# Performance work log

Hardware: AMD Instinct MI355X
Metric: run time of the kernel (lower is better)

## Reference

```python
import jax, jax.numpy as jnp
import numpy as np

B, L, H, T = 32, 512, 768, 8  # batch, tokens, dim_hidden, num_trees
DK = H // T


def setup_inputs() -> dict:
    key = jax.random.key(0)
    ks = jax.random.split(key, 8)
    s = 1.0 / np.sqrt(H)
    return {
        "input": jax.random.normal(ks[0], (B, L, H), dtype=jnp.float32),
        "src_mask": jax.random.randint(ks[1], (B, L), 0, 2, dtype=jnp.int32),
        "Wq": jax.random.uniform(ks[2], (H, H), minval=-s, maxval=s, dtype=jnp.float32),
        "bq": jax.random.uniform(ks[3], (H,), minval=-s, maxval=s, dtype=jnp.float32),
        "Wk": jax.random.uniform(ks[4], (H, H), minval=-s, maxval=s, dtype=jnp.float32),
        "bk": jax.random.uniform(ks[5], (H,), minval=-s, maxval=s, dtype=jnp.float32),
        "Wroot": jax.random.uniform(ks[6], (T, H), minval=-s, maxval=s, dtype=jnp.float32),
        "broot": jax.random.uniform(ks[7], (T,), minval=-s, maxval=s, dtype=jnp.float32),
    }


def reference(input, src_mask, Wq, bq, Wk, bk, Wroot, broot):
    x = input
    # multi-head attention probabilities (eval mode, no dropout)
    q = (x @ Wq.T + bq).reshape(B, L, T, DK).transpose(0, 2, 1, 3)  # (B,T,L,DK)
    k = (x @ Wk.T + bk).reshape(B, L, T, DK).transpose(0, 2, 1, 3)
    scores = jnp.einsum("btqd,btkd->btqk", q, k) / jnp.sqrt(jnp.float32(DK))
    scores = jnp.where(src_mask[:, None, None, :] == 0, -1e9, scores)
    p_attn = jax.nn.softmax(scores, axis=-1)  # (B,T,L,L) == f_ij per tree

    # root scores f_i per tree: (B,T,L)
    f = jnp.einsum("blh,th->btl", x, Wroot) + broot[None, :, None]

    eye = jnp.eye(L, dtype=x.dtype)
    A = jnp.exp(p_attn) * (1.0 - eye)           # zero diagonal
    deg = A.sum(axis=2)                          # column sums (dim=1 per tree)
    Lap = -A + deg[..., None, :] * eye           # Laplacian, deg on diagonal
    Lbar = Lap.at[:, :, 0, :].set(f)             # replace first row with root scores

    LLinv = jnp.linalg.inv(Lbar)                 # (B,T,L,L)
    d0 = f * LLinv[..., 0]                       # f_i * LLinv[:, :, 0]  -> (B,T,L)
    diag = jnp.diagonal(LLinv, axis1=-2, axis2=-1)  # (B,T,L)
    tmp1 = A * diag[..., None, :]                # A[i,j] * LLinv[j,j]
    tmp2 = A * jnp.swapaxes(LLinv, -1, -2)       # A[i,j] * LLinv[j,i]
    col_mask = (jnp.arange(L) != 0).astype(x.dtype)[None, None, None, :]  # zero first col
    row_mask = (jnp.arange(L) != 0).astype(x.dtype)[None, None, :, None]  # zero first row
    dx = col_mask * tmp1 - row_mask * tmp2       # (B,T,L,L)

    d = jnp.concatenate([d0[..., None, :], dx], axis=-2)  # (B,T,L+1,L)
    df = jnp.swapaxes(d, -1, -2)                 # (B,T,L,L+1)
    att = df[..., 1:]                            # (B,T,L,L); stacked adj_list
    return att
```

## Files before the change

### kernel.cpp

```cpp
#include <hip/hip_runtime.h>
#include <math.h>

#define NB_ 64
#define NPH 8

__global__ __launch_bounds__(256) void proj_gemm(const float* __restrict__ x,
    const float* __restrict__ Wq, const float* __restrict__ bq,
    const float* __restrict__ Wk, const float* __restrict__ bk,
    float* __restrict__ Qb, float* __restrict__ Kb) {
  const float* W    = blockIdx.z ? Wk : Wq;
  const float* bias = blockIdx.z ? bk : bq;
  float* out        = blockIdx.z ? Kb : Qb;
  const int m0 = blockIdx.x * 128;
  const int n0 = blockIdx.y * 64;
  __shared__ float Xs[16][132];
  __shared__ float Ws[16][68];
  const int tid = threadIdx.x;
  const int tm = tid & 15, tn = tid >> 4;
  float acc[8][4];
#pragma unroll
  for (int i = 0; i < 8; i++)
#pragma unroll
    for (int j = 0; j < 4; j++) acc[i][j] = 0.f;

  for (int kk = 0; kk < 768; kk += 16) {
#pragma unroll
    for (int rep = 0; rep < 2; rep++) {
      int fidx = tid + rep * 256;
      int row = fidx >> 2, f4i = fidx & 3;
      float4 v = ((const float4*)(x + (size_t)(m0 + row) * 768 + kk))[f4i];
      Xs[f4i * 4 + 0][row] = v.x; Xs[f4i * 4 + 1][row] = v.y;
      Xs[f4i * 4 + 2][row] = v.z; Xs[f4i * 4 + 3][row] = v.w;
    }
    { int row = tid >> 2, f4i = tid & 3;
      float4 v = ((const float4*)(W + (size_t)(n0 + row) * 768 + kk))[f4i];
      Ws[f4i * 4 + 0][row] = v.x; Ws[f4i * 4 + 1][row] = v.y;
      Ws[f4i * 4 + 2][row] = v.z; Ws[f4i * 4 + 3][row] = v.w;
    }
    __syncthreads();
#pragma unroll
    for (int k = 0; k < 16; k++) {
      float4 a0 = *(const float4*)&Xs[k][tm * 4];
      float4 a1 = *(const float4*)&Xs[k][tm * 4 + 64];
      float4 bv = *(const float4*)&Ws[k][tn * 4];
      float am[8] = {a0.x,a0.y,a0.z,a0.w,a1.x,a1.y,a1.z,a1.w};
      float bn[4] = {bv.x,bv.y,bv.z,bv.w};
#pragma unroll
      for (int i = 0; i < 8; i++)
#pragma unroll
        for (int j = 0; j < 4; j++) acc[i][j] += am[i] * bn[j];
    }
    __syncthreads();
  }
  float b0 = bias[n0 + tn * 4 + 0], b1 = bias[n0 + tn * 4 + 1];
  float b2 = bias[n0 + tn * 4 + 2], b3 = bias[n0 + tn * 4 + 3];
#pragma unroll
  for (int i = 0; i < 4; i++) {
    float4 o = {acc[i][0] + b0, acc[i][1] + b1, acc[i][2] + b2, acc[i][3] + b3};
    *(float4*)(out + (size_t)(m0 + tm * 4 + i) * 768 + n0 + tn * 4) = o;
    float4 o2 = {acc[i+4][0] + b0, acc[i+4][1] + b1, acc[i+4][2] + b2, acc[i+4][3] + b3};
    *(float4*)(out + (size_t)(m0 + 64 + tm * 4 + i) * 768 + n0 + tn * 4) = o2;
  }
}

__global__ __launch_bounds__(256) void f_kernel(const float* __restrict__ x,
    const float* __restrict__ Wroot, const float* __restrict__ broot,
    float* __restrict__ fout) {
  int row = blockIdx.x * 256 + threadIdx.x;
  int b = row >> 9, l = row & 511;
  float acc[8] = {0,0,0,0,0,0,0,0};
  const float4* xr = (const float4*)(x + (size_t)row * 768);
  for (int h4 = 0; h4 < 192; h4++) {
    float4 xv = xr[h4];
#pragma unroll
    for (int t = 0; t < 8; t++) {
      float4 wv = ((const float4*)(Wroot + (size_t)t * 768))[h4];
      acc[t] += xv.x * wv.x + xv.y * wv.y + xv.z * wv.z + xv.w * wv.w;
    }
  }
#pragma unroll
  for (int t = 0; t < 8; t++)
    fout[(size_t)((b * 8 + t) << 9) + l] = acc[t] + broot[t];
}

__global__ __launch_bounds__(256) void scores_kernel(const float* __restrict__ Qb,
    const float* __restrict__ Kb, const int* __restrict__ mask,
    float* __restrict__ A) {
  const int lin = blockIdx.x;
  const int xcd = lin & 7;
  const int idx = lin >> 3;
  const int bt  = xcd * 32 + (idx >> 5);
  const int q0  = (idx & 31) * 16;
  const int b = bt >> 3, t = bt & 7;
  __shared__ float  S[16][512];
  __shared__ float4 Qs4[16][24];
  __shared__ float  part[16][16];
  __shared__ float  invsum[16];
  const int tid = threadIdx.x;
  for (int i = tid; i < 384; i += 256) {
    int q = i / 24, f4 = i % 24;
    Qs4[q][f4] =
        ((const float4*)(Qb + (size_t)(b * 512 + q0 + q) * 768 + t * 96))[f4];
  }
  __syncthreads();
  const float scl = 0.10206207261596575f;
#pragma unroll 1
  for (int rep = 0; rep < 2; rep++) {
    const int k = rep * 256 + tid;
    const float4* kr = (const float4*)(Kb + (size_t)(b * 512 + k) * 768 + t * 96);
    float acc[16];
#pragma unroll
    for (int q = 0; q < 16; q++) acc[q] = 0.f;
#pragma unroll 4
    for (int f4 = 0; f4 < 24; f4++) {
      float4 kv = kr[f4];
#pragma unroll
      for (int q = 0; q < 16; q++) {
        float4 qv = Qs4[q][f4];
        acc[q] += qv.x * kv.x + qv.y * kv.y + qv.z * kv.z + qv.w * kv.w;
      }
    }
    int mk = mask[b * 512 + k];
#pragma unroll
    for (int q = 0; q < 16; q++)
      S[q][k] = mk ? expf(acc[q] * scl) : 0.f;
  }
  __syncthreads();
  { int q = tid >> 4, j = tid & 15;
    float s = 0.f;
#pragma unroll
    for (int i = 0; i < 32; i++) s += S[q][j + 16 * i];
    part[q][j] = s; }
  __syncthreads();
  if (tid < 16) {
    float s = 0.f;
#pragma unroll
    for (int j = 0; j < 16; j++) s += part[tid][j];
    invsum[tid] = 1.f / fmaxf(s, 1e-30f);
  }
  __syncthreads();
#pragma unroll 1
  for (int rep = 0; rep < 2; rep++) {
    const int k = rep * 256 + tid;
#pragma unroll
    for (int q = 0; q < 16; q++) {
      float p = S[q][k] * invsum[q];
      float a = (q0 + q == k) ? 0.f : expf(p);
      A[(size_t)(bt * 512 + q0 + q) * 512 + k] = a;
    }
  }
}

__global__ __launch_bounds__(256) void deg_kernel(const float* __restrict__ A,
                                                  float* __restrict__ deg) {
  int bt = blockIdx.y, k = blockIdx.x * 256 + threadIdx.x;
  const float* Ab = A + (size_t)bt * 262144;
  float s = 0.f;
  for (int q = 0; q < 512; q++) s += Ab[(size_t)q * 512 + k];
  deg[bt * 512 + k] = s;
}

__global__ __launch_bounds__(128) void build_kernel(const float* __restrict__ A,
    const float* __restrict__ fin, const float* __restrict__ deg,
    float* __restrict__ M) {
  int q = blockIdx.x, bt = blockIdx.y, tid = threadIdx.x;
  size_t base = (size_t)bt * 262144;
  float4* Mo = (float4*)(M + base + (size_t)q * 512);
  if (q == 0) {
    Mo[tid] = ((const float4*)(fin + (size_t)bt * 512))[tid];
  } else {
    float4 a = ((const float4*)(A + base + (size_t)q * 512))[tid];
    float4 m = {-a.x, -a.y, -a.z, -a.w};
    int k0 = tid * 4;
    if (q >= k0 && q < k0 + 4) {
      float d = deg[bt * 512 + q];
      if      (q == k0    ) m.x += d;
      else if (q == k0 + 1) m.y += d;
      else if (q == k0 + 2) m.z += d;
      else                  m.w += d;
    }
    Mo[tid] = m;
  }
}

__global__ __launch_bounds__(512) void panel_kernel(float* __restrict__ M,
                                                    int* __restrict__ pivr, int ph) {
  const int bt = blockIdx.x, tid = threadIdx.x;
  const int j0 = ph * NB_;
  __shared__ float rowj[NB_];
  __shared__ float bufj[NB_], bufr[NB_];
  __shared__ float pivval_s;
  __shared__ unsigned long long wred[8];
  __shared__ int pivlist[NB_];
  float* Mb = M + (size_t)bt * 262144;
  float r[NB_];
  {
    const float4* p0 = (const float4*)(Mb + (size_t)tid * 512 + j0);
#pragma unroll
    for (int fi = 0; fi < 16; fi++) {
      float4 a = p0[fi];
      r[4*fi] = a.x; r[4*fi+1] = a.y; r[4*fi+2] = a.z; r[4*fi+3] = a.w;
    }
  }
  const int lane = tid & 63, wv = tid >> 6;
  for (int l = 0; l < NB_; l++) {
    const int j = j0 + l;
    float v = 0.f;
#pragma unroll
    for (int c = 0; c < NB_; c++) v = (c == l) ? r[c] : v;
    float best = -1.f; int bidx = 0;
    if (tid >= j) { best = fabsf(v); bidx = tid; }
    unsigned long long pk = (best >= 0.f)
        ? ((((unsigned long long)__float_as_uint(best)) << 32) | (unsigned)bidx) : 0ull;
#pragma unroll
    for (int off = 32; off > 0; off >>= 1) {
      unsigned long long o = __shfl_xor(pk, off, 64);
      if (o > pk) pk = o;
    }
    if (lane == 0) wred[wv] = pk;
    __syncthreads();
    unsigned long long ma = wred[0];
#pragma unroll
    for (int w = 1; w < 8; w++) ma = (wred[w] > ma) ? wred[w] : ma;
    const int rr = (int)(unsigned)(ma & 0xffffffffull);
    if (tid == rr) {
      pivval_s = v;
#pragma unroll
      for (int c = 0; c < NB_; c++) bufr[c] = r[c];
    }
    if (tid == j) {
#pragma unroll
      for (int c = 0; c < NB_; c++) bufj[c] = r[c];
    }
    if (tid == 0) pivlist[l] = rr;
    __syncthreads();
    const float rinv = 1.f / pivval_s;
    if (tid == j) {
#pragma unroll
      for (int c = 0; c < NB_; c++) {
        float nv = (c == l) ? rinv : bufr[c] * rinv;
        r[c] = nv;
        rowj[c] = nv;
      }
    }
    if (rr != j && tid == rr) {
#pragma unroll
      for (int c = 0; c < NB_; c++) r[c] = bufj[c];
    }
    __syncthreads();
    if (tid != j) {
      float m = 0.f;
#pragma unroll
      for (int c = 0; c < NB_; c++) m = (c == l) ? r[c] : m;
#pragma unroll
      for (int c = 0; c < NB_; c++) r[c] = ((c == l) ? 0.f : r[c]) - m * rowj[c];
    }
    __syncthreads();
  }
  {
    float4* p0 = (float4*)(Mb + (size_t)tid * 512 + j0);
#pragma unroll
    for (int fi = 0; fi < 16; fi++) {
      float4 a = {r[4*fi], r[4*fi+1], r[4*fi+2], r[4*fi+3]};
      p0[fi] = a;
    }
  }
  if (tid < NB_) pivr[bt * 512 + j0 + tid] = pivlist[tid];
}

__global__ __launch_bounds__(256) void stage_kernel(const float* __restrict__ M,
    const int* __restrict__ pivr, float* __restrict__ Stg,
    int* __restrict__ rowslot, int ph) {
  const int bt = blockIdx.x, tid = threadIdx.x;
  const int j0 = ph * NB_;
  __shared__ int perm_s[512];
  __shared__ int srcrow[128];
  __shared__ int cnt;
  const float* Mb = M + (size_t)bt * 262144;
  float* Sb = Stg + (size_t)bt * 98304;
  int* rsb = rowslot + bt * 512;
  for (int i = tid; i < 512; i += 256) perm_s[i] = i;
  if (tid == 0) cnt = 0;
  __syncthreads();
  if (tid == 0) {
    for (int l = 0; l < NB_; l++) {
      int r = pivr[bt * 512 + j0 + l];
      int tp = perm_s[j0 + l]; perm_s[j0 + l] = perm_s[r]; perm_s[r] = tp;
    }
  }
  __syncthreads();
  for (int i = tid; i < 512; i += 256) {
    int s = -1;
    if (perm_s[i] != i) { s = atomicAdd(&cnt, 1); srcrow[s] = perm_s[i]; }
    rsb[i] = s;
  }
  __syncthreads();
  const int nmv = cnt;
  for (int idx = tid; idx < 64 * 128; idx += 256) {
    int l = idx >> 7, f4 = idx & 127;
    ((float4*)(Sb + (size_t)l * 512))[f4] =
        ((const float4*)(Mb + (size_t)perm_s[j0 + l] * 512))[f4];
  }
  for (int idx = tid; idx < nmv * 128; idx += 256) {
    int s = idx >> 7, f4 = idx & 127;
    ((float4*)(Sb + (size_t)(64 + s) * 512))[f4] =
        ((const float4*)(Mb + (size_t)srcrow[s] * 512))[f4];
  }
}

__global__ __launch_bounds__(256) void update_kernel(float* __restrict__ M,
    const float* __restrict__ Stg, const int* __restrict__ rowslot, int ph) {
  const int lin = blockIdx.x;
  const int xcd = lin & 7;
  const int idx = lin >> 3;
  const int bt  = xcd * 32 + (idx / 28);
  const int tl  = idx % 28;
  const int rt  = tl / 7;
  int ct = tl % 7;
  ct += (ct >= ph) ? 1 : 0;
  const int i0 = rt * 128, c0 = ct * 64;
  const int j0 = ph * NB_;
  float* Mb = M + (size_t)bt * 262144;
  const float* Sb = Stg + (size_t)bt * 98304;
  __shared__ float Vs[16][132];
  __shared__ float Xs[16][68];
  __shared__ int rs_s[128];
  const int tid = threadIdx.x;
  const int tm = tid & 15, tn = tid >> 4;
  if (tid < 128) rs_s[tid] = rowslot[bt * 512 + i0 + tid];
  float acc[8][4];
#pragma unroll
  for (int i = 0; i < 8; i++)
#pragma unroll
    for (int j = 0; j < 4; j++) acc[i][j] = 0.f;

#pragma unroll 1
  for (int kk = 0; kk < 64; kk += 16) {
#pragma unroll
    for (int rep = 0; rep < 2; rep++) {
      int fidx = tid + rep * 256;
      int row = fidx >> 2, f4i = fidx & 3;
      float4 v = *(const float4*)(Mb + (size_t)(i0 + row) * 512 + j0 + kk + f4i * 4);
      Vs[f4i * 4 + 0][row] = v.x; Vs[f4i * 4 + 1][row] = v.y;
      Vs[f4i * 4 + 2][row] = v.z; Vs[f4i * 4 + 3][row] = v.w;
    }
    {
      int row = tid >> 4, f4i = tid & 15;
      float4 v = *(const float4*)(Sb + (size_t)(kk + row) * 512 + c0 + f4i * 4);
      *(float4*)&Xs[row][f4i * 4] = v;
    }
    __syncthreads();
#pragma unroll
    for (int k = 0; k < 16; k++) {
      float4 a0 = *(const float4*)&Vs[k][tm * 4];
      float4 a1 = *(const float4*)&Vs[k][tm * 4 + 64];
      float4 bv = *(const float4*)&Xs[k][tn * 4];
      float am[8] = {a0.x,a0.y,a0.z,a0.w,a1.x,a1.y,a1.z,a1.w};
      float bn[4] = {bv.x,bv.y,bv.z,bv.w};
#pragma unroll
      for (int i = 0; i < 8; i++)
#pragma unroll
        for (int j = 0; j < 4; j++) acc[i][j] += am[i] * bn[j];
    }
    __syncthreads();
  }
  const int colg = c0 + tn * 4;
#pragma unroll
  for (int half = 0; half < 2; half++)
#pragma unroll
    for (int i = 0; i < 4; i++) {
      const int rl = half * 64 + tm * 4 + i;
      const int row = i0 + rl;
      const int rs = rs_s[rl];
      const float* oldp = (rs >= 0) ? (Sb + (size_t)(64 + rs) * 512 + colg)
                                    : (Mb + (size_t)row * 512 + colg);
      float4 o = *(const float4*)oldp;
      o.x += acc[half*4+i][0]; o.y += acc[half*4+i][1];
      o.z += acc[half*4+i][2]; o.w += acc[half*4+i][3];
      if (row >= j0 && row < j0 + NB_) {
        float4 xr = *(const float4*)(Sb + (size_t)(row - j0) * 512 + colg);
        o.x -= xr.x; o.y -= xr.y; o.z -= xr.z; o.w -= xr.w;
      }
      *(float4*)(Mb + (size_t)row * 512 + colg) = o;
    }
}

__global__ __launch_bounds__(64) void colsrc_kernel(const float* __restrict__ M,
    const int* __restrict__ pivr, int* __restrict__ colsrc, float* __restrict__ diagv) {
  const int bt = blockIdx.x, tid = threadIdx.x;
  __shared__ int piv[512];
  __shared__ int cs[512];
  for (int i = tid; i < 512; i += 64) { piv[i] = pivr[bt * 512 + i]; cs[i] = i; }
  __syncthreads();
  if (tid == 0) {
    for (int j = 511; j >= 0; j--) { int r = piv[j]; int tp = cs[j]; cs[j] = cs[r]; cs[r] = tp; }
  }
  __syncthreads();
  const float* Mb = M + (size_t)bt * 262144;
  for (int i = tid; i < 512; i += 64) {
    colsrc[bt * 512 + i] = cs[i];
    diagv[bt * 512 + i] = Mb[(size_t)i * 512 + cs[i]];
  }
}

__global__ __launch_bounds__(256) void final_kernel(const float* __restrict__ M,
    const int* __restrict__ colsrc, const float* __restrict__ diagv,
    float* __restrict__ Aout) {
  const int bt = blockIdx.y;
  int x = blockIdx.x, ti = 0;
  while (x >= 8 - ti) { x -= 8 - ti; ti++; }
  const int tj = ti + x;
  const int tid = threadIdx.x, c = tid & 63, g = tid >> 6;
  __shared__ float Aa[64][65];
  __shared__ float Ab[64][65];
  __shared__ int csj[64], csi[64];
  __shared__ float dgi[64], dgj[64];
  const size_t base = (size_t)bt * 262144;
  const float* Mb = M + base;
  float* Ao = Aout + base;
  if (tid < 64)       { csj[tid] = colsrc[bt * 512 + tj * 64 + tid];
                        dgi[tid] = diagv[bt * 512 + ti * 64 + tid]; }
  else if (tid < 128) { int u = tid - 64;
                        csi[u] = colsrc[bt * 512 + ti * 64 + u];
                        dgj[u] = diagv[bt * 512 + tj * 64 + u]; }
  for (int rr = g; rr < 64; rr += 4)
    Aa[rr][c] = Ao[(size_t)(tj * 64 + rr) * 512 + ti * 64 + c];
  if (ti != tj)
    for (int rr = g; rr < 64; rr += 4)
      Ab[rr][c] = Ao[(size_t)(ti * 64 + rr) * 512 + tj * 64 + c];
  __syncthreads();
  for (int kk = g; kk < 64; kk += 4) {
    int krow = ti * 64 + kk, q = tj * 64 + c;
    float a = Aa[c][kk];
    float llv = Mb[(size_t)krow * 512 + csj[c]];
    float val = 0.f;
    if (krow != 0) val = a * dgi[kk];
    if (q != 0)    val -= a * llv;
    Ao[(size_t)krow * 512 + q] = val;
  }
  if (ti != tj) {
    for (int kk = g; kk < 64; kk += 4) {
      int krow = tj * 64 + kk, q = ti * 64 + c;
      float a = Ab[c][kk];
      float llv = Mb[(size_t)krow * 512 + csi[c]];
      float val = 0.f;
      if (krow != 0) val = a * dgj[kk];
      if (q != 0)    val -= a * llv;
      Ao[(size_t)krow * 512 + q] = val;
    }
  }
}

extern "C" void kernel_launch(void* const* d_in, const int* in_sizes, int n_in,
                              void* d_out, int out_size, void* d_ws, size_t ws_size,
                              hipStream_t stream) {
  const float* x     = (const float*)d_in[0];
  const int*   mask  = (const int*)d_in[1];
  const float* Wq    = (const float*)d_in[2];
  const float* bq    = (const float*)d_in[3];
  const float* Wk    = (const float*)d_in[4];
  const float* bk    = (const float*)d_in[5];
  const float* Wroot = (const float*)d_in[6];
  const float* broot = (const float*)d_in[7];
  float* A = (float*)d_out;

  float* ws = (float*)d_ws;
  size_t off = 0;
  float* M    = ws + off; off += (size_t)256 * 512 * 512;
  float* Qb   = ws + off; off += (size_t)16384 * 768;
  float* Kb   = ws + off; off += (size_t)16384 * 768;
  float* fbuf = ws + off; off += (size_t)256 * 512;
  float* deg  = ws + off; off += (size_t)256 * 512;
  float* dgv  = ws + off; off += (size_t)256 * 512;
  int* pivr   = (int*)(ws + off); off += (size_t)256 * 512;
  int* csrc   = (int*)(ws + off); off += (size_t)256 * 512;
  int* rslot  = (int*)(ws + off); off += (size_t)256 * 512;
  if (ws_size < off * sizeof(float)) return;

  float* Stg = Qb;

  proj_gemm<<<dim3(128, 12, 2), 256, 0, stream>>>(x, Wq, bq, Wk, bk, Qb, Kb);
  f_kernel<<<64, 256, 0, stream>>>(x, Wroot, broot, fbuf);
  scores_kernel<<<dim3(8192), 256, 0, stream>>>(Qb, Kb, mask, A);
  deg_kernel<<<dim3(2, 256), 256, 0, stream>>>(A, deg);
  build_kernel<<<dim3(512, 256), 128, 0, stream>>>(A, fbuf, deg, M);
  for (int ph = 0; ph < NPH; ph++) {
    panel_kernel<<<256, 512, 0, stream>>>(M, pivr, ph);
    stage_kernel<<<256, 256, 0, stream>>>(M, pivr, Stg, rslot, ph);
    update_kernel<<<dim3(7168), 256, 0, stream>>>(M, Stg, rslot, ph);
  }
  colsrc_kernel<<<256, 64, 0, stream>>>(M, pivr, csrc, dgv);
  final_kernel<<<dim3(36, 256), 256, 0, stream>>>(M, csrc, dgv, A);
}
```

Before: 4.536 ms.

## Fuse deg into build, stage into panel, widen GEMM tile, pre-permute columns

Widens the projection GEMM tile to 128x128 per block for more register reuse. Fuses the column-sum degree computation into the Laplacian build so A is read once, and folds the row-staging step into the panel kernel to drop one launch per phase. Adds a permute pass that reorders LU-inverse columns in place so the final kernel reads contiguous data instead of gathering. This trades an extra full-matrix pass for coalesced final reads and higher register pressure in the GEMM.

```diff
diff --git a/kernel.cpp b/kernel.cpp
--- a/kernel.cpp
+++ b/kernel.cpp
@@ -12,16 +12,16 @@
   const float* bias = blockIdx.z ? bk : bq;
   float* out        = blockIdx.z ? Kb : Qb;
   const int m0 = blockIdx.x * 128;
-  const int n0 = blockIdx.y * 64;
+  const int n0 = blockIdx.y * 128;
   __shared__ float Xs[16][132];
-  __shared__ float Ws[16][68];
+  __shared__ float Ws2[16][132];
   const int tid = threadIdx.x;
   const int tm = tid & 15, tn = tid >> 4;
-  float acc[8][4];
+  float acc[8][8];
 #pragma unroll
   for (int i = 0; i < 8; i++)
 #pragma unroll
-    for (int j = 0; j < 4; j++) acc[i][j] = 0.f;
+    for (int j = 0; j < 8; j++) acc[i][j] = 0.f;
 
   for (int kk = 0; kk < 768; kk += 16) {
 #pragma unroll
@@ -32,35 +32,48 @@
       Xs[f4i * 4 + 0][row] = v.x; Xs[f4i * 4 + 1][row] = v.y;
       Xs[f4i * 4 + 2][row] = v.z; Xs[f4i * 4 + 3][row] = v.w;
     }
-    { int row = tid >> 2, f4i = tid & 3;
+#pragma unroll
+    for (int rep = 0; rep < 2; rep++) {
+      int fidx = tid + rep * 256;
+      int row = fidx >> 2, f4i = fidx & 3;
       float4 v = ((const float4*)(W + (size_t)(n0 + row) * 768 + kk))[f4i];
-      Ws[f4i * 4 + 0][row] = v.x; Ws[f4i * 4 + 1][row] = v.y;
-      Ws[f4i * 4 + 2][row] = v.z; Ws[f4i * 4 + 3][row] = v.w;
+      Ws2[f4i * 4 + 0][row] = v.x; Ws2[f4i * 4 + 1][row] = v.y;
+      Ws2[f4i * 4 + 2][row] = v.z; Ws2[f4i * 4 + 3][row] = v.w;
     }
     __syncthreads();
 #pragma unroll
     for (int k = 0; k < 16; k++) {
       float4 a0 = *(const float4*)&Xs[k][tm * 4];
       float4 a1 = *(const float4*)&Xs[k][tm * 4 + 64];
-      float4 bv = *(const float4*)&Ws[k][tn * 4];
+      float4 b0 = *(const float4*)&Ws2[k][tn * 4];
+      float4 b1 = *(const float4*)&Ws2[k][tn * 4 + 64];
       float am[8] = {a0.x,a0.y,a0.z,a0.w,a1.x,a1.y,a1.z,a1.w};
-      float bn[4] = {bv.x,bv.y,bv.z,bv.w};
+      float bn[8] = {b0.x,b0.y,b0.z,b0.w,b1.x,b1.y,b1.z,b1.w};
 #pragma unroll
       for (int i = 0; i < 8; i++)
 #pragma unroll
-        for (int j = 0; j < 4; j++) acc[i][j] += am[i] * bn[j];
-    }
-    __syncthreads();
-  }
-  float b0 = bias[n0 + tn * 4 + 0], b1 = bias[n0 + tn * 4 + 1];
-  float b2 = bias[n0 + tn * 4 + 2], b3 = bias[n0 + tn * 4 + 3];
-#pragma unroll
-  for (int i = 0; i < 4; i++) {
-    float4 o = {acc[i][0] + b0, acc[i][1] + b1, acc[i][2] + b2, acc[i][3] + b3};
-    *(float4*)(out + (size_t)(m0 + tm * 4 + i) * 768 + n0 + tn * 4) = o;
-    float4 o2 = {acc[i+4][0] + b0, acc[i+4][1] + b1, acc[i+4][2] + b2, acc[i+4][3] + b3};
-    *(float4*)(out + (size_t)(m0 + 64 + tm * 4 + i) * 768 + n0 + tn * 4) = o2;
-  }
+        for (int j = 0; j < 8; j++) acc[i][j] += am[i] * bn[j];
+    }
+    __syncthreads();
+  }
+  float bA[4], bB[4];
+#pragma unroll
+  for (int j = 0; j < 4; j++) {
+    bA[j] = bias[n0 + tn * 4 + j];
+    bB[j] = bias[n0 + 64 + tn * 4 + j];
+  }
+#pragma unroll
+  for (int half = 0; half < 2; half++)
+#pragma unroll
+    for (int i = 0; i < 4; i++) {
+      const int row = m0 + half * 64 + tm * 4 + i;
+      float4 oA = {acc[half*4+i][0] + bA[0], acc[half*4+i][1] + bA[1],
+                   acc[half*4+i][2] + bA[2], acc[half*4+i][3] + bA[3]};
+      *(float4*)(out + (size_t)row * 768 + n0 + tn * 4) = oA;
+      float4 oB = {acc[half*4+i][4] + bB[0], acc[half*4+i][5] + bB[1],
+                   acc[half*4+i][6] + bB[2], acc[half*4+i][7] + bB[3]};
+      *(float4*)(out + (size_t)row * 768 + n0 + 64 + tn * 4) = oB;
+    }
 }
 
 __global__ __launch_bounds__(256) void f_kernel(const float* __restrict__ x,
@@ -151,40 +164,25 @@
   }
 }
 
-__global__ __launch_bounds__(256) void deg_kernel(const float* __restrict__ A,
-                                                  float* __restrict__ deg) {
-  int bt = blockIdx.y, k = blockIdx.x * 256 + threadIdx.x;
+__global__ __launch_bounds__(256) void build_kernel(const float* __restrict__ A,
+    const float* __restrict__ fin, float* __restrict__ M) {
+  const int bt = blockIdx.y;
+  const int k = blockIdx.x * 256 + threadIdx.x;
   const float* Ab = A + (size_t)bt * 262144;
+  float* Mb = M + (size_t)bt * 262144;
   float s = 0.f;
-  for (int q = 0; q < 512; q++) s += Ab[(size_t)q * 512 + k];
-  deg[bt * 512 + k] = s;
-}
-
-__global__ __launch_bounds__(128) void build_kernel(const float* __restrict__ A,
-    const float* __restrict__ fin, const float* __restrict__ deg,
-    float* __restrict__ M) {
-  int q = blockIdx.x, bt = blockIdx.y, tid = threadIdx.x;
-  size_t base = (size_t)bt * 262144;
-  float4* Mo = (float4*)(M + base + (size_t)q * 512);
-  if (q == 0) {
-    Mo[tid] = ((const float4*)(fin + (size_t)bt * 512))[tid];
-  } else {
-    float4 a = ((const float4*)(A + base + (size_t)q * 512))[tid];
-    float4 m = {-a.x, -a.y, -a.z, -a.w};
-    int k0 = tid * 4;
-    if (q >= k0 && q < k0 + 4) {
-      float d = deg[bt * 512 + q];
-      if      (q == k0    ) m.x += d;
-      else if (q == k0 + 1) m.y += d;
-      else if (q == k0 + 2) m.z += d;
-      else                  m.w += d;
-    }
-    Mo[tid] = m;
-  }
+  { float a = Ab[k]; s += a; Mb[k] = fin[bt * 512 + k]; }
+  for (int q = 1; q < 512; q++) {
+    float a = Ab[(size_t)q * 512 + k];
+    s += a;
+    Mb[(size_t)q * 512 + k] = -a;
+  }
+  if (k != 0) Mb[(size_t)k * 512 + k] = s;
 }
 
 __global__ __launch_bounds__(512) void panel_kernel(float* __restrict__ M,
-                                                    int* __restrict__ pivr, int ph) {
+    int* __restrict__ pivr, float* __restrict__ Stg, int* __restrict__ rowslot,
+    int ph) {
   const int bt = blockIdx.x, tid = threadIdx.x;
   const int j0 = ph * NB_;
   __shared__ float rowj[NB_];
@@ -192,6 +190,9 @@
   __shared__ float pivval_s;
   __shared__ unsigned long long wred[8];
   __shared__ int pivlist[NB_];
+  __shared__ int perm_s[512];
+  __shared__ int srcrow[128];
+  __shared__ int cnt;
   float* Mb = M + (size_t)bt * 262144;
   float r[NB_];
   {
@@ -266,42 +267,31 @@
     }
   }
   if (tid < NB_) pivr[bt * 512 + j0 + tid] = pivlist[tid];
-}
-
-__global__ __launch_bounds__(256) void stage_kernel(const float* __restrict__ M,
-    const int* __restrict__ pivr, float* __restrict__ Stg,
-    int* __restrict__ rowslot, int ph) {
-  const int bt = blockIdx.x, tid = threadIdx.x;
-  const int j0 = ph * NB_;
-  __shared__ int perm_s[512];
-  __shared__ int srcrow[128];
-  __shared__ int cnt;
-  const float* Mb = M + (size_t)bt * 262144;
-  float* Sb = Stg + (size_t)bt * 98304;
-  int* rsb = rowslot + bt * 512;
-  for (int i = tid; i < 512; i += 256) perm_s[i] = i;
+
+  if (tid < 512) perm_s[tid] = tid;
   if (tid == 0) cnt = 0;
   __syncthreads();
   if (tid == 0) {
     for (int l = 0; l < NB_; l++) {
-      int r = pivr[bt * 512 + j0 + l];
-      int tp = perm_s[j0 + l]; perm_s[j0 + l] = perm_s[r]; perm_s[r] = tp;
-    }
-  }
-  __syncthreads();
-  for (int i = tid; i < 512; i += 256) {
+      int rw = pivlist[l];
+      int tp = perm_s[j0 + l]; perm_s[j0 + l] = perm_s[rw]; perm_s[rw] = tp;
+    }
+  }
+  __syncthreads();
+  {
     int s = -1;
-    if (perm_s[i] != i) { s = atomicAdd(&cnt, 1); srcrow[s] = perm_s[i]; }
-    rsb[i] = s;
+    if (perm_s[tid] != tid) { s = atomicAdd(&cnt, 1); srcrow[s] = perm_s[tid]; }
+    rowslot[bt * 512 + tid] = s;
   }
   __syncthreads();
   const int nmv = cnt;
-  for (int idx = tid; idx < 64 * 128; idx += 256) {
+  float* Sb = Stg + (size_t)bt * 98304;
+  for (int idx = tid; idx < 64 * 128; idx += 512) {
     int l = idx >> 7, f4 = idx & 127;
     ((float4*)(Sb + (size_t)l * 512))[f4] =
         ((const float4*)(Mb + (size_t)perm_s[j0 + l] * 512))[f4];
   }
-  for (int idx = tid; idx < nmv * 128; idx += 256) {
+  for (int idx = tid; idx < nmv * 128; idx += 512) {
     int s = idx >> 7, f4 = idx & 127;
     ((float4*)(Sb + (size_t)(64 + s) * 512))[f4] =
         ((const float4*)(Mb + (size_t)srcrow[s] * 512))[f4];
@@ -385,8 +375,8 @@
     }
 }
 
-__global__ __launch_bounds__(64) void colsrc_kernel(const float* __restrict__ M,
-    const int* __restrict__ pivr, int* __restrict__ colsrc, float* __restrict__ diagv) {
+__global__ __launch_bounds__(64) void colsrc_kernel(const int* __restrict__ pivr,
+                                                    int* __restrict__ colsrc) {
   const int bt = blockIdx.x, tid = threadIdx.x;
   __shared__ int piv[512];
   __shared__ int cs[512];
@@ -396,16 +386,44 @@
     for (int j = 511; j >= 0; j--) { int r = piv[j]; int tp = cs[j]; cs[j] = cs[r]; cs[r] = tp; }
   }
   __syncthreads();
-  const float* Mb = M + (size_t)bt * 262144;
-  for (int i = tid; i < 512; i += 64) {
-    colsrc[bt * 512 + i] = cs[i];
-    diagv[bt * 512 + i] = Mb[(size_t)i * 512 + cs[i]];
+  for (int i = tid; i < 512; i += 64) colsrc[bt * 512 + i] = cs[i];
+}
+
+__global__ __launch_bounds__(256) void permute_kernel(float* __restrict__ M,
+    const int* __restrict__ colsrc, float* __restrict__ diagv) {
+  const int bt = blockIdx.y, r0 = blockIdx.x * 32;
+  __shared__ int cs[512];
+  __shared__ float rowbuf[4][512];
+  const int tid = threadIdx.x;
+  const int lane = tid & 63, w = tid >> 6;
+  for (int i = tid; i < 512; i += 256) cs[i] = colsrc[bt * 512 + i];
+  __syncthreads();
+  float* Mb = M + (size_t)bt * 262144;
+  for (int it = 0; it < 8; it++) {
+    const int row = r0 + it * 4 + w;
+    float4 v0 = ((const float4*)(Mb + (size_t)row * 512))[lane];
+    float4 v1 = ((const float4*)(Mb + (size_t)row * 512))[lane + 64];
+    *(float4*)&rowbuf[w][lane * 4] = v0;
+    *(float4*)&rowbuf[w][256 + lane * 4] = v1;
+    __syncthreads();
+    float o[8];
+#pragma unroll
+    for (int j = 0; j < 8; j++) o[j] = rowbuf[w][cs[lane * 8 + j]];
+    if ((row >> 3) == lane) {
+#pragma unroll
+      for (int j = 0; j < 8; j++)
+        if ((row & 7) == j) diagv[bt * 512 + row] = o[j];
+    }
+    float4 oA = {o[0], o[1], o[2], o[3]};
+    float4 oB = {o[4], o[5], o[6], o[7]};
+    *(float4*)(Mb + (size_t)row * 512 + lane * 8) = oA;
+    *(float4*)(Mb + (size_t)row * 512 + lane * 8 + 4) = oB;
+    __syncthreads();
   }
 }
 
 __global__ __launch_bounds__(256) void final_kernel(const float* __restrict__ M,
-    const int* __restrict__ colsrc, const float* __restrict__ diagv,
-    float* __restrict__ Aout) {
+    const float* __restrict__ diagv, float* __restrict__ Aout) {
   const int bt = blockIdx.y;
   int x = blockIdx.x, ti = 0;
   while (x >= 8 - ti) { x -= 8 - ti; ti++; }
@@ -413,16 +431,12 @@
   const int tid = threadIdx.x, c = tid & 63, g = tid >> 6;
   __shared__ float Aa[64][65];
   __shared__ float Ab[64][65];
-  __shared__ int csj[64], csi[64];
   __shared__ float dgi[64], dgj[64];
   const size_t base = (size_t)bt * 262144;
   const float* Mb = M + base;
   float* Ao = Aout + base;
-  if (tid < 64)       { csj[tid] = colsrc[bt * 512 + tj * 64 + tid];
-                        dgi[tid] = diagv[bt * 512 + ti * 64 + tid]; }
-  else if (tid < 128) { int u = tid - 64;
-                        csi[u] = colsrc[bt * 512 + ti * 64 + u];
-                        dgj[u] = diagv[bt * 512 + tj * 64 + u]; }
+  if (tid < 64)       dgi[tid] = diagv[bt * 512 + ti * 64 + tid];
+  else if (tid < 128) dgj[tid - 64] = diagv[bt * 512 + tj * 64 + (tid - 64)];
   for (int rr = g; rr < 64; rr += 4)
     Aa[rr][c] = Ao[(size_t)(tj * 64 + rr) * 512 + ti * 64 + c];
   if (ti != tj)
@@ -432,7 +446,7 @@
   for (int kk = g; kk < 64; kk += 4) {
     int krow = ti * 64 + kk, q = tj * 64 + c;
     float a = Aa[c][kk];
-    float llv = Mb[(size_t)krow * 512 + csj[c]];
+    float llv = Mb[(size_t)krow * 512 + q];
     float val = 0.f;
     if (krow != 0) val = a * dgi[kk];
     if (q != 0)    val -= a * llv;
@@ -442,7 +456,7 @@
     for (int kk = g; kk < 64; kk += 4) {
       int krow = tj * 64 + kk, q = ti * 64 + c;
       float a = Ab[c][kk];
-      float llv = Mb[(size_t)krow * 512 + csi[c]];
+      float llv = Mb[(size_t)krow * 512 + q];
       float val = 0.f;
       if (krow != 0) val = a * dgj[kk];
       if (q != 0)    val -= a * llv;
@@ -470,7 +484,6 @@
   float* Qb   = ws + off; off += (size_t)16384 * 768;
   float* Kb   = ws + off; off += (size_t)16384 * 768;
   float* fbuf = ws + off; off += (size_t)256 * 512;
-  float* deg  = ws + off; off += (size_t)256 * 512;
   float* dgv  = ws + off; off += (size_t)256 * 512;
   int* pivr   = (int*)(ws + off); off += (size_t)256 * 512;
   int* csrc   = (int*)(ws + off); off += (size_t)256 * 512;
@@ -479,16 +492,15 @@
 
   float* Stg = Qb;
 
-  proj_gemm<<<dim3(128, 12, 2), 256, 0, stream>>>(x, Wq, bq, Wk, bk, Qb, Kb);
+  proj_gemm<<<dim3(128, 6, 2), 256, 0, stream>>>(x, Wq, bq, Wk, bk, Qb, Kb);
   f_kernel<<<64, 256, 0, stream>>>(x, Wroot, broot, fbuf);
   scores_kernel<<<dim3(8192), 256, 0, stream>>>(Qb, Kb, mask, A);
-  deg_kernel<<<dim3(2, 256), 256, 0, stream>>>(A, deg);
-  build_kernel<<<dim3(512, 256), 128, 0, stream>>>(A, fbuf, deg, M);
+  build_kernel<<<dim3(2, 256), 256, 0, stream>>>(A, fbuf, M);
   for (int ph = 0; ph < NPH; ph++) {
-    panel_kernel<<<256, 512, 0, stream>>>(M, pivr, ph);
-    stage_kernel<<<256, 256, 0, stream>>>(M, pivr, Stg, rslot, ph);
+    panel_kernel<<<256, 512, 0, stream>>>(M, pivr, Stg, rslot, ph);
     update_kernel<<<dim3(7168), 256, 0, stream>>>(M, Stg, rslot, ph);
   }
-  colsrc_kernel<<<256, 64, 0, stream>>>(M, pivr, csrc, dgv);
-  final_kernel<<<dim3(36, 256), 256, 0, stream>>>(M, csrc, dgv, A);
-}
+  colsrc_kernel<<<256, 64, 0, stream>>>(pivr, csrc);
+  permute_kernel<<<dim3(16, 256), 256, 0, stream>>>(M, csrc, dgv);
+  final_kernel<<<dim3(36, 256), 256, 0, stream>>>(M, dgv, A);
+}
```

Result: no change. 4.478 ms (-1.3%).
